# Kernel tuning notes

Measured on AMD Instinct MI355X. Metric: run time of the kernel, lower is better.

Reference implementation:

```python
import jax, jax.numpy as jnp
import numpy as np

NUM_HEADS = 16
HEAD_DIM = 128
ROTARY_DIM = 32  # head_dim * rotary_pct(0.25)
ROPE_BASE = 10000.0
SCALE = HEAD_DIM ** -0.5


def _rotate_half(x):
    x1, x2 = jnp.split(x, 2, axis=-1)
    return jnp.concatenate((-x2, x1), axis=-1)


def _rope_tables(seq_len, dtype):
    inv_freq = 1.0 / (ROPE_BASE ** (jnp.arange(0, ROTARY_DIM, 2, dtype=jnp.float32) / ROTARY_DIM))
    freqs = jnp.arange(seq_len, dtype=jnp.float32)[:, None] * inv_freq[None, :]  # [S, rd/2]
    emb = jnp.concatenate((freqs, freqs), axis=-1)  # [S, rd]
    return jnp.cos(emb).astype(dtype), jnp.sin(emb).astype(dtype)


def setup_inputs() -> dict:
    key = jax.random.key(0)
    k1, k2, k3 = jax.random.split(key, 3)
    B, S, H = 2, 2048, 2048
    hidden_states = jax.random.normal(k1, (B, S, H), dtype=jnp.float32)
    attention_mask = jnp.zeros((B, 1, S, S), dtype=jnp.float32)
    Wqkv = jax.random.normal(k2, (H, 3 * H), dtype=jnp.float32) * (H ** -0.5)
    Wout = jax.random.normal(k3, (H, H), dtype=jnp.float32) * (H ** -0.5)
    return {"hidden_states": hidden_states, "attention_mask": attention_mask,
            "Wqkv": Wqkv, "Wout": Wout}


def reference(hidden_states, attention_mask, Wqkv, Wout):
    B, S, H = hidden_states.shape
    qkv = jnp.einsum('bsh,hk->bsk', hidden_states, Wqkv)  # [B,S,3H]
    q, k, v = jnp.split(qkv, 3, axis=-1)

    def to_heads(x):
        return x.reshape(B, S, NUM_HEADS, HEAD_DIM).transpose(0, 2, 1, 3)  # [B,nh,S,hd]

    q, k, v = to_heads(q), to_heads(k), to_heads(v)

    cos, sin = _rope_tables(S, hidden_states.dtype)  # [S, ROTARY_DIM]
    cos = cos[None, None, :, :]
    sin = sin[None, None, :, :]

    def rope(x):
        xr = x[..., :ROTARY_DIM]
        xr = xr * cos + _rotate_half(xr) * sin
        return jnp.concatenate((xr, x[..., ROTARY_DIM:]), axis=-1)

    q, k = rope(q), rope(k)

    scores = jnp.einsum('bhqd,bhkd->bhqk', q, k) * SCALE + attention_mask
    probs = jax.nn.softmax(scores, axis=-1)  # dropout p=0 -> identity
    ctx = jnp.einsum('bhqk,bhkd->bhqd', probs, v)
    ctx = ctx.transpose(0, 2, 1, 3).reshape(B, S, H)
    return jnp.einsum('bsh,ho->bso', ctx, Wout)
```

## Files before the change

kernel.cpp:

```cpp
#include <hip/hip_runtime.h>

typedef __attribute__((ext_vector_type(4))) float f32x4;
typedef __attribute__((ext_vector_type(8))) short s16x8;
typedef __attribute__((ext_vector_type(4))) unsigned short u16x4;
typedef __attribute__((ext_vector_type(8))) unsigned short u16x8;

#define DEVINL __device__ __forceinline__

constexpr int Bb = 2;
constexpr int Ss = 2048;
constexpr int Hh = 2048;
constexpr int NH = 16;
constexpr int HD = 128;
constexpr float ATT_SCALE = 0.08838834764831845f;
constexpr float CEXP = ATT_SCALE * 1.44269504089f;
constexpr float INV_SCALE = 11.313708498984761f;
constexpr float RAW_THR = 90.50966799f;

DEVINL unsigned short f2bf(float f) {
    unsigned u = __float_as_uint(f);
    u += 0x7FFFu + ((u >> 16) & 1u);
    return (unsigned short)(u >> 16);
}
DEVINL float bf2f(unsigned short h) { return __uint_as_float(((unsigned)h) << 16); }
DEVINL float fexp2(float x) { return __builtin_amdgcn_exp2f(x); }

DEVINL void gl16(const void* g, void* l) {
    __builtin_amdgcn_global_load_lds((const __attribute__((address_space(1))) void*)g,
                                     (__attribute__((address_space(3))) void*)l, 16, 0, 0);
}

__global__ void zero_flag_k(int* f) { if (threadIdx.x == 0) *f = 0; }

__global__ void scan_mask_k(const float* __restrict__ m, int* __restrict__ flag) {
    size_t i = ((size_t)blockIdx.x * 256 + threadIdx.x) * 4;
    f32x4 v = *(const f32x4*)(m + i);
    int any = (v[0] != 0.f) || (v[1] != 0.f) || (v[2] != 0.f) || (v[3] != 0.f);
    if (__any(any)) { if ((threadIdx.x & 63) == 0) atomicOr(flag, 1); }
}

__global__ void convH_k(const float* __restrict__ x, unsigned short* __restrict__ y) {
    size_t i = (size_t)blockIdx.x * 256 + threadIdx.x;
    f32x4 a = *(const f32x4*)(x + i * 8);
    f32x4 b = *(const f32x4*)(x + i * 8 + 4);
    u16x8 o;
    o[0] = f2bf(a[0]); o[1] = f2bf(a[1]); o[2] = f2bf(a[2]); o[3] = f2bf(a[3]);
    o[4] = f2bf(b[0]); o[5] = f2bf(b[1]); o[6] = f2bf(b[2]); o[7] = f2bf(b[3]);
    *(u16x8*)(y + i * 8) = o;
}

__global__ void convT_k(const float* __restrict__ W, unsigned short* __restrict__ Wt,
                        int R, int C) {
    __shared__ float tile[32][33];
    int c0 = blockIdx.x * 32, r0 = blockIdx.y * 32;
    int t = threadIdx.x;
    int rr = t >> 3, cc = (t & 7) * 4;
    f32x4 v = *(const f32x4*)(W + (size_t)(r0 + rr) * C + c0 + cc);
    tile[rr][cc + 0] = v[0]; tile[rr][cc + 1] = v[1];
    tile[rr][cc + 2] = v[2]; tile[rr][cc + 3] = v[3];
    __syncthreads();
    u16x4 o;
    o[0] = f2bf(tile[cc + 0][rr]); o[1] = f2bf(tile[cc + 1][rr]);
    o[2] = f2bf(tile[cc + 2][rr]); o[3] = f2bf(tile[cc + 3][rr]);
    *(u16x4*)(Wt + (size_t)(c0 + rr) * R + r0 + cc) = o;
}

template<int MODE>
__global__ __launch_bounds__(256)
void gemm_bt_k(const unsigned short* __restrict__ A, const unsigned short* __restrict__ Bt,
               float* __restrict__ Cf, unsigned short* __restrict__ Cb,
               int M, int N, int K) {
    __shared__ char lds[128 * 64 * 2 * 2];
    char* As = lds;
    char* Bs = lds + 128 * 64 * 2;
    int t = threadIdx.x, w = t >> 6, ln = t & 63, lr = ln & 15, lg = ln >> 4;
    int f = blockIdx.x;
    int cpx = gridDim.x >> 3;
    int s = (f & 7) * cpx + (f >> 3);
    int nbn = N >> 7;
    int nb = s % nbn, mb = s / nbn;
    int m0 = mb * 128, n0 = nb * 128;
    int wr = w >> 1, wc = w & 1;
    const char* Abt = (const char*)A;
    const char* Bbt = (const char*)Bt;

    f32x4 acc[4][4];
#pragma unroll
    for (int i = 0; i < 4; ++i)
#pragma unroll
        for (int j = 0; j < 4; ++j) { acc[i][j][0] = 0.f; acc[i][j][1] = 0.f; acc[i][j][2] = 0.f; acc[i][j][3] = 0.f; }

    for (int k0 = 0; k0 < K; k0 += 64) {
        __syncthreads();
#pragma unroll
        for (int vv = 0; vv < 4; ++vv) {
            int ci = vv * 256 + t;
            int row = ci >> 3, cb = (ci & 7) << 4;
            int sc = cb ^ ((row & 7) << 4);
            gl16(Abt + ((size_t)(m0 + row) * K + k0) * 2 + sc, As + ci * 16);
            gl16(Bbt + ((size_t)(n0 + row) * K + k0) * 2 + sc, Bs + ci * 16);
        }
        __syncthreads();
#pragma unroll
        for (int kc = 0; kc < 2; ++kc) {
            s16x8 af[4], bfr[4];
#pragma unroll
            for (int i = 0; i < 4; ++i) {
                int rowa = wr * 64 + i * 16 + lr;
                af[i] = *(const s16x8*)(As + rowa * 128 + ((kc * 64 + lg * 16) ^ ((rowa & 7) << 4)));
                int rowb = wc * 64 + i * 16 + lr;
                bfr[i] = *(const s16x8*)(Bs + rowb * 128 + ((kc * 64 + lg * 16) ^ ((rowb & 7) << 4)));
            }
#pragma unroll
            for (int i = 0; i < 4; ++i)
#pragma unroll
                for (int j = 0; j < 4; ++j)
                    acc[i][j] = __builtin_amdgcn_mfma_f32_16x16x32_bf16(af[i], bfr[j], acc[i][j], 0, 0, 0);
        }
    }

    if (MODE == 0 && n0 < 4096 && wc == 0) {
        float invf = fexp2((float)lr * -0.83048202372f);
#pragma unroll
        for (int i = 0; i < 4; ++i)
#pragma unroll
            for (int r = 0; r < 4; ++r) {
                int srow = (m0 + wr * 64 + i * 16 + lg * 4 + r) & (Ss - 1);
                float sn, cs;
                sincosf((float)srow * invf, &sn, &cs);
                float x1 = acc[i][0][r], x2 = acc[i][1][r];
                acc[i][0][r] = x1 * cs - x2 * sn;
                acc[i][1][r] = x2 * cs + x1 * sn;
            }
    }

#pragma unroll
    for (int i = 0; i < 4; ++i)
#pragma unroll
        for (int j = 0; j < 4; ++j)
#pragma unroll
            for (int r = 0; r < 4; ++r) {
                int gr = m0 + wr * 64 + i * 16 + lg * 4 + r;
                int gc = n0 + wc * 64 + j * 16 + lr;
                float vv = acc[i][j][r];
                if (MODE == 1) Cf[(size_t)gr * N + gc] = vv;
                else           Cb[(size_t)gr * N + gc] = f2bf(vv);
            }
}

__global__ void vtrans_k(const unsigned short* __restrict__ qkv, unsigned short* __restrict__ Vt) {
    __shared__ unsigned short tile[64][40];
    int bh = blockIdx.x; int b = bh >> 4, h = bh & 15;
    int s0 = blockIdx.y * 64, d0 = blockIdx.z * 32;
    int t = threadIdx.x;
    int r = t >> 2, c8 = (t & 3) * 8;
    u16x8 v = *(const u16x8*)(qkv + ((size_t)(b * Ss + s0 + r)) * 6144 + 4096 + h * 128 + d0 + c8);
#pragma unroll
    for (int e = 0; e < 8; ++e) tile[r][c8 + e] = v[e];
    __syncthreads();
    int dr = t >> 3, sc = (t & 7) * 8;
    u16x8 o;
#pragma unroll
    for (int e = 0; e < 8; ++e) o[e] = tile[sc + e][dr];
    *(u16x8*)(Vt + ((size_t)bh * HD + d0 + dr) * Ss + s0 + sc) = o;
}

__global__ __launch_bounds__(512)
void attn_k(const unsigned short* __restrict__ qkv, const unsigned short* __restrict__ Vt,
            const float* __restrict__ mask, unsigned short* __restrict__ ctxb,
            const int* __restrict__ flag) {
    __shared__ char ldsK[64 * 256];
    __shared__ char ldsV[128 * 128];
    __shared__ unsigned short ldsP[8][1024];
    int f = blockIdx.x;
    int swzb = (f & 7) * 64 + (f >> 3);
    int bh = swzb >> 4, qt = swzb & 15;
    int b = bh >> 4, h = bh & 15;
    int t = threadIdx.x, w = t >> 6, ln = t & 63, lr = ln & 15, lg = ln >> 4;
    int useMask = *flag;
    int qw0 = qt * 128 + w * 16;
    const char* qkvB = (const char*)qkv;
    const char* VtB = (const char*)Vt;

    s16x8 qf[4];
    size_t qbase = ((size_t)(b * Ss + qw0 + lr)) * 6144 + h * 128;
#pragma unroll
    for (int kc = 0; kc < 4; ++kc) qf[kc] = *(const s16x8*)(qkv + qbase + kc * 32 + lg * 8);

    float mr = -3e38f, lsum = 0.f;
    f32x4 ctxa[8];
#pragma unroll
    for (int dn = 0; dn < 8; ++dn) { ctxa[dn][0] = 0.f; ctxa[dn][1] = 0.f; ctxa[dn][2] = 0.f; ctxa[dn][3] = 0.f; }
    const float* mrow = mask + (size_t)b * Ss * Ss;

    for (int kk0 = 0; kk0 < Ss; kk0 += 64) {
        __syncthreads();
#pragma unroll
        for (int c = 0; c < 2; ++c) {
            int ci = c * 512 + t;
            int krow = ci >> 4, kcb = (ci & 15) << 4;
            gl16(qkvB + (((size_t)(b * Ss + kk0 + krow)) * 6144 + 2048 + h * 128) * 2 + (kcb ^ ((krow & 7) << 4)),
                 ldsK + ci * 16);
            int vrow = ci >> 3, vcb = (ci & 7) << 4;
            gl16(VtB + (((size_t)(bh * 128 + vrow)) * 2048 + kk0) * 2 + (vcb ^ ((vrow & 7) << 4)),
                 ldsV + ci * 16);
        }
        __syncthreads();

        f32x4 st[4];
#pragma unroll
        for (int n = 0; n < 4; ++n) {
            f32x4 sacc = {0.f, 0.f, 0.f, 0.f};
            const char* kb = ldsK + (n * 16 + lr) * 256;
            int sw = (lr & 7) << 4;
#pragma unroll
            for (int kc = 0; kc < 4; ++kc) {
                s16x8 kf = *(const s16x8*)(kb + ((kc * 64 + lg * 16) ^ sw));
                sacc = __builtin_amdgcn_mfma_f32_16x16x32_bf16(kf, qf[kc], sacc, 0, 0, 0);
            }
            st[n] = sacc;
        }
        if (useMask) {
#pragma unroll
            for (int n = 0; n < 4; ++n)
#pragma unroll
                for (int r = 0; r < 4; ++r)
                    st[n][r] += mrow[(size_t)(qw0 + lr) * Ss + kk0 + n * 16 + lg * 4 + r] * INV_SCALE;
        }
        float pmax = st[0][0];
#pragma unroll
        for (int n = 0; n < 4; ++n)
#pragma unroll
            for (int r = 0; r < 4; ++r) pmax = fmaxf(pmax, st[n][r]);
        pmax = fmaxf(pmax, __shfl_xor(pmax, 16));
        pmax = fmaxf(pmax, __shfl_xor(pmax, 32));
        bool need = pmax > mr + RAW_THR;
        if (__any(need)) {
            float mn = fmaxf(mr, pmax);
            float al = fexp2((mr - mn) * CEXP);
            mr = mn;
            lsum *= al;
            float a0 = __shfl(al, lg * 4 + 0), a1 = __shfl(al, lg * 4 + 1);
            float a2 = __shfl(al, lg * 4 + 2), a3 = __shfl(al, lg * 4 + 3);
#pragma unroll
            for (int dn = 0; dn < 8; ++dn) {
                ctxa[dn][0] *= a0; ctxa[dn][1] *= a1; ctxa[dn][2] *= a2; ctxa[dn][3] *= a3;
            }
        }
        float mC = mr * CEXP;
        float rs = 0.f;
        u16x4 pk[4];
#pragma unroll
        for (int n = 0; n < 4; ++n)
#pragma unroll
            for (int r = 0; r < 4; ++r) {
                float p = fexp2(st[n][r] * CEXP - mC);
                rs += p;
                pk[n][r] = f2bf(p);
            }
        rs += __shfl_xor(rs, 16);
        rs += __shfl_xor(rs, 32);
        lsum += rs;
        char* pw = (char*)ldsP[w];
        int swp = (lr & 7) << 4;
#pragma unroll
        for (int n = 0; n < 4; ++n)
            *(u16x4*)(pw + lr * 128 + ((32 * n + 8 * lg) ^ swp)) = pk[n];
        asm volatile("s_waitcnt lgkmcnt(0)" ::: "memory");
        s16x8 pa[2];
#pragma unroll
        for (int c2 = 0; c2 < 2; ++c2)
            pa[c2] = *(const s16x8*)(pw + lr * 128 + ((64 * c2 + 16 * lg) ^ swp));
#pragma unroll
        for (int dn = 0; dn < 8; ++dn) {
            const char* vb = ldsV + (dn * 16 + lr) * 128;
#pragma unroll
            for (int c2 = 0; c2 < 2; ++c2) {
                s16x8 vf = *(const s16x8*)(vb + ((c2 * 64 + lg * 16) ^ swp));
                ctxa[dn] = __builtin_amdgcn_mfma_f32_16x16x32_bf16(pa[c2], vf, ctxa[dn], 0, 0, 0);
            }
        }
    }
    float l0 = 1.f / __shfl(lsum, lg * 4 + 0), l1 = 1.f / __shfl(lsum, lg * 4 + 1);
    float l2 = 1.f / __shfl(lsum, lg * 4 + 2), l3 = 1.f / __shfl(lsum, lg * 4 + 3);
#pragma unroll
    for (int dn = 0; dn < 8; ++dn) {
        size_t base = ((size_t)(b * Ss + qw0)) * Hh + h * 128 + dn * 16 + lr;
        ctxb[base + (size_t)(lg * 4 + 0) * Hh] = f2bf(ctxa[dn][0] * l0);
        ctxb[base + (size_t)(lg * 4 + 1) * Hh] = f2bf(ctxa[dn][1] * l1);
        ctxb[base + (size_t)(lg * 4 + 2) * Hh] = f2bf(ctxa[dn][2] * l2);
        ctxb[base + (size_t)(lg * 4 + 3) * Hh] = f2bf(ctxa[dn][3] * l3);
    }
}

extern "C" void kernel_launch(void* const* d_in, const int* in_sizes, int n_in,
                              void* d_out, int out_size, void* d_ws, size_t ws_size,
                              hipStream_t stream) {
    (void)in_sizes; (void)n_in; (void)out_size; (void)ws_size;
    const float* hidden = (const float*)d_in[0];
    const float* mask   = (const float*)d_in[1];
    const float* Wqkv   = (const float*)d_in[2];
    const float* Wout   = (const float*)d_in[3];
    float* out = (float*)d_out;

    char* ws = (char*)d_ws;
    size_t off = 0;
    auto alloc = [&](size_t bytes) { char* p = ws + off; off += (bytes + 255) & ~(size_t)255; return p; };
    unsigned short* hbf   = (unsigned short*)alloc((size_t)8388608 * 2);
    unsigned short* wqkvT = (unsigned short*)alloc((size_t)12582912 * 2);
    unsigned short* woutT = (unsigned short*)alloc((size_t)4194304 * 2);
    unsigned short* qkv   = (unsigned short*)alloc((size_t)25165824 * 2);
    unsigned short* Vt    = (unsigned short*)alloc((size_t)8388608 * 2);
    int* flag             = (int*)alloc(256);
    unsigned short* ctx = hbf;

    zero_flag_k<<<1, 64, 0, stream>>>(flag);
    scan_mask_k<<<2048, 256, 0, stream>>>(mask, flag);
    convH_k<<<4096, 256, 0, stream>>>(hidden, hbf);
    convT_k<<<dim3(192, 64), 256, 0, stream>>>(Wqkv, wqkvT, 2048, 6144);
    convT_k<<<dim3(64, 64), 256, 0, stream>>>(Wout, woutT, 2048, 2048);
    gemm_bt_k<0><<<1536, 256, 0, stream>>>(hbf, wqkvT, nullptr, qkv, 4096, 6144, 2048);
    vtrans_k<<<dim3(32, 32, 4), 256, 0, stream>>>(qkv, Vt);
    attn_k<<<512, 512, 0, stream>>>(qkv, Vt, mask, ctx, flag);
    gemm_bt_k<1><<<512, 256, 0, stream>>>(ctx, woutT, out, nullptr, 4096, 2048, 2048);
}
```

Measured before the change: 314.8 us.

## Use 256x256 double-buffered GEMM tiles with overlapped global-to-LDS loads

Replaces the 128x128 single-buffered GEMM with a 256x256 tile kernel using 512 threads. It double-buffers LDS at 128KB and issues the next K-tile's global loads while the current MFMAs run, with explicit waitcnt, barriers and setprio around the MFMA bursts. This aims to raise data reuse per tile and hide memory latency behind compute. In exchange, the grids shrink to 384 and 128 blocks, which risks wave-quantization tails and leaves many CUs idle for the output projection. The large LDS footprint also limits each CU to one block.

```diff
diff --git a/kernel.cpp b/kernel.cpp
--- a/kernel.cpp
+++ b/kernel.cpp
@@ -66,66 +66,114 @@
 }
 
 template<int MODE>
-__global__ __launch_bounds__(256)
-void gemm_bt_k(const unsigned short* __restrict__ A, const unsigned short* __restrict__ Bt,
+__global__ __launch_bounds__(512, 2)
+void gemm256_k(const unsigned short* __restrict__ A, const unsigned short* __restrict__ Bt,
                float* __restrict__ Cf, unsigned short* __restrict__ Cb,
                int M, int N, int K) {
-    __shared__ char lds[128 * 64 * 2 * 2];
-    char* As = lds;
-    char* Bs = lds + 128 * 64 * 2;
+    __shared__ char lds[131072];
     int t = threadIdx.x, w = t >> 6, ln = t & 63, lr = ln & 15, lg = ln >> 4;
-    int f = blockIdx.x;
-    int cpx = gridDim.x >> 3;
+    int wm = w >> 2, wn = w & 3;
+    int f = blockIdx.x, cpx = gridDim.x >> 3;
     int s = (f & 7) * cpx + (f >> 3);
-    int nbn = N >> 7;
+    int nbn = N >> 8;
     int nb = s % nbn, mb = s / nbn;
-    int m0 = mb * 128, n0 = nb * 128;
-    int wr = w >> 1, wc = w & 1;
-    const char* Abt = (const char*)A;
-    const char* Bbt = (const char*)Bt;
-
-    f32x4 acc[4][4];
-#pragma unroll
-    for (int i = 0; i < 4; ++i)
+    int m0 = mb * 256, n0 = nb * 256;
+    const char* Ab = (const char*)A;
+    const char* Bbp = (const char*)Bt;
+
+    f32x4 acc[8][4];
+#pragma unroll
+    for (int i = 0; i < 8; ++i)
 #pragma unroll
         for (int j = 0; j < 4; ++j) { acc[i][j][0] = 0.f; acc[i][j][1] = 0.f; acc[i][j][2] = 0.f; acc[i][j][3] = 0.f; }
 
-    for (int k0 = 0; k0 < K; k0 += 64) {
-        __syncthreads();
-#pragma unroll
-        for (int vv = 0; vv < 4; ++vv) {
-            int ci = vv * 256 + t;
+    auto STAGE = [&](int buf, int kt) {
+        size_t k0 = (size_t)kt * 64;
+        char* dA = lds + buf * 65536;
+        char* dB = dA + 32768;
+#pragma unroll
+        for (int ld = 0; ld < 4; ++ld) {
+            int ci = ld * 512 + t;
             int row = ci >> 3, cb = (ci & 7) << 4;
             int sc = cb ^ ((row & 7) << 4);
-            gl16(Abt + ((size_t)(m0 + row) * K + k0) * 2 + sc, As + ci * 16);
-            gl16(Bbt + ((size_t)(n0 + row) * K + k0) * 2 + sc, Bs + ci * 16);
-        }
-        __syncthreads();
-#pragma unroll
-        for (int kc = 0; kc < 2; ++kc) {
-            s16x8 af[4], bfr[4];
-#pragma unroll
-            for (int i = 0; i < 4; ++i) {
-                int rowa = wr * 64 + i * 16 + lr;
-                af[i] = *(const s16x8*)(As + rowa * 128 + ((kc * 64 + lg * 16) ^ ((rowa & 7) << 4)));
-                int rowb = wc * 64 + i * 16 + lr;
-                bfr[i] = *(const s16x8*)(Bs + rowb * 128 + ((kc * 64 + lg * 16) ^ ((rowb & 7) << 4)));
-            }
-#pragma unroll
-            for (int i = 0; i < 4; ++i)
+            gl16(Ab + ((size_t)(m0 + row) * K + k0) * 2 + sc, dA + ci * 16);
+        }
+#pragma unroll
+        for (int ld = 0; ld < 4; ++ld) {
+            int ci = ld * 512 + t;
+            int row = ci >> 3, cb = (ci & 7) << 4;
+            int sc = cb ^ ((row & 7) << 4);
+            gl16(Bbp + ((size_t)(n0 + row) * K + k0) * 2 + sc, dB + ci * 16);
+        }
+    };
+
+    const int NT = K >> 6;
+    STAGE(0, 0);
+    STAGE(1, 1);
+
+    for (int it = 0; it < (NT >> 1); ++it) {
+        int e = 2 * it;
+#pragma unroll
+        for (int half = 0; half < 2; ++half) {
+            const char* Ax = lds + half * 65536;
+            const char* Bx = Ax + 32768;
+            asm volatile("s_waitcnt vmcnt(8)" ::: "memory");
+            __builtin_amdgcn_s_barrier();
+            __builtin_amdgcn_sched_barrier(0);
+            s16x8 af[8], bfr[4];
+#pragma unroll
+            for (int i = 0; i < 8; ++i) {
+                int rowa = wm * 128 + i * 16 + lr;
+                af[i] = *(const s16x8*)(Ax + rowa * 128 + ((lg * 16) ^ ((rowa & 7) << 4)));
+            }
+#pragma unroll
+            for (int j = 0; j < 4; ++j) {
+                int rowb = wn * 64 + j * 16 + lr;
+                bfr[j] = *(const s16x8*)(Bx + rowb * 128 + ((lg * 16) ^ ((rowb & 7) << 4)));
+            }
+            asm volatile("s_waitcnt lgkmcnt(0)" ::: "memory");
+            __builtin_amdgcn_sched_barrier(0);
+            __builtin_amdgcn_s_setprio(1);
+#pragma unroll
+            for (int i = 0; i < 8; ++i)
 #pragma unroll
                 for (int j = 0; j < 4; ++j)
                     acc[i][j] = __builtin_amdgcn_mfma_f32_16x16x32_bf16(af[i], bfr[j], acc[i][j], 0, 0, 0);
+            __builtin_amdgcn_s_setprio(0);
+#pragma unroll
+            for (int i = 0; i < 8; ++i) {
+                int rowa = wm * 128 + i * 16 + lr;
+                af[i] = *(const s16x8*)(Ax + rowa * 128 + ((64 + lg * 16) ^ ((rowa & 7) << 4)));
+            }
+#pragma unroll
+            for (int j = 0; j < 4; ++j) {
+                int rowb = wn * 64 + j * 16 + lr;
+                bfr[j] = *(const s16x8*)(Bx + rowb * 128 + ((64 + lg * 16) ^ ((rowb & 7) << 4)));
+            }
+            asm volatile("s_waitcnt lgkmcnt(0)" ::: "memory");
+            __builtin_amdgcn_sched_barrier(0);
+            __builtin_amdgcn_s_barrier();
+            __builtin_amdgcn_sched_barrier(0);
+            int stg = e + 2 + half;
+            if (stg >= NT) stg -= 2;
+            STAGE(half, stg);
+            __builtin_amdgcn_s_setprio(1);
+#pragma unroll
+            for (int i = 0; i < 8; ++i)
+#pragma unroll
+                for (int j = 0; j < 4; ++j)
+                    acc[i][j] = __builtin_amdgcn_mfma_f32_16x16x32_bf16(af[i], bfr[j], acc[i][j], 0, 0, 0);
+            __builtin_amdgcn_s_setprio(0);
         }
     }
 
-    if (MODE == 0 && n0 < 4096 && wc == 0) {
+    if (MODE == 0 && n0 < 4096 && (wn & 1) == 0) {
         float invf = fexp2((float)lr * -0.83048202372f);
 #pragma unroll
-        for (int i = 0; i < 4; ++i)
+        for (int i = 0; i < 8; ++i)
 #pragma unroll
             for (int r = 0; r < 4; ++r) {
-                int srow = (m0 + wr * 64 + i * 16 + lg * 4 + r) & (Ss - 1);
+                int srow = (m0 + wm * 128 + i * 16 + lg * 4 + r) & (Ss - 1);
                 float sn, cs;
                 sincosf((float)srow * invf, &sn, &cs);
                 float x1 = acc[i][0][r], x2 = acc[i][1][r];
@@ -135,13 +183,13 @@
     }
 
 #pragma unroll
-    for (int i = 0; i < 4; ++i)
+    for (int i = 0; i < 8; ++i)
 #pragma unroll
         for (int j = 0; j < 4; ++j)
 #pragma unroll
             for (int r = 0; r < 4; ++r) {
-                int gr = m0 + wr * 64 + i * 16 + lg * 4 + r;
-                int gc = n0 + wc * 64 + j * 16 + lr;
+                int gr = m0 + wm * 128 + i * 16 + lg * 4 + r;
+                int gc = n0 + wn * 64 + j * 16 + lr;
                 float vv = acc[i][j][r];
                 if (MODE == 1) Cf[(size_t)gr * N + gc] = vv;
                 else           Cb[(size_t)gr * N + gc] = f2bf(vv);
@@ -319,8 +367,8 @@
     convH_k<<<4096, 256, 0, stream>>>(hidden, hbf);
     convT_k<<<dim3(192, 64), 256, 0, stream>>>(Wqkv, wqkvT, 2048, 6144);
     convT_k<<<dim3(64, 64), 256, 0, stream>>>(Wout, woutT, 2048, 2048);
-    gemm_bt_k<0><<<1536, 256, 0, stream>>>(hbf, wqkvT, nullptr, qkv, 4096, 6144, 2048);
+    gemm256_k<0><<<384, 512, 0, stream>>>(hbf, wqkvT, nullptr, qkv, 4096, 6144, 2048);
     vtrans_k<<<dim3(32, 32, 4), 256, 0, stream>>>(qkv, Vt);
     attn_k<<<512, 512, 0, stream>>>(qkv, Vt, mask, ctx, flag);
-    gemm_bt_k<1><<<512, 256, 0, stream>>>(ctx, woutT, out, nullptr, 4096, 2048, 2048);
-}
+    gemm256_k<1><<<128, 512, 0, stream>>>(ctx, woutT, out, nullptr, 4096, 2048, 2048);
+}
```

Measured after the change: 315.1 us. Within noise of the previous version (+0.1%).

## Replace QKV projection GEMM with 256x256-tile pipelined kernel

Applied to the files above, without the earlier changes.

Adds a new GEMM kernel using 256x256 output tiles, 512 threads and a double-buffered LDS pipeline. Global-to-LDS loads for upcoming K-slices are interleaved with MFMA phases under explicit waitcnt, barriers and priority hints. It is used for the QKV projection with the fused RoPE epilogue, replacing the 128x128 kernel. The aim is more operand reuse per byte loaded and better overlap of memory and compute. The cost is heavy register and LDS pressure (128 KB LDS, launch_bounds 512,2) and only 384 blocks, which can hurt occupancy or tail balance.

```diff
diff --git a/kernel.cpp b/kernel.cpp
--- a/kernel.cpp
+++ b/kernel.cpp
@@ -63,6 +63,127 @@
     o[0] = f2bf(tile[cc + 0][rr]); o[1] = f2bf(tile[cc + 1][rr]);
     o[2] = f2bf(tile[cc + 2][rr]); o[3] = f2bf(tile[cc + 3][rr]);
     *(u16x4*)(Wt + (size_t)(c0 + rr) * R + r0 + cc) = o;
+}
+
+#define PH(buf, kh, ih, sbuf, sX, skh, st, vm)                                    \
+  {                                                                               \
+    const char* Ar = lds + (buf)*65536 + (kh)*16384;                              \
+    const char* Br = lds + (buf)*65536 + 32768 + (kh)*16384;                      \
+    s16x8 af[4];                                                                  \
+    if ((ih) == 0) {                                                              \
+      _Pragma("unroll")                                                           \
+      for (int j = 0; j < 4; ++j)                                                 \
+        bfr[j] = *(const s16x8*)(Br + (wn*64 + j*16 + lr)*64 + lg*16);            \
+    }                                                                             \
+    _Pragma("unroll")                                                             \
+    for (int i = 0; i < 4; ++i)                                                   \
+      af[i] = *(const s16x8*)(Ar + (wm*128 + (ih)*64 + i*16 + lr)*64 + lg*16);    \
+    STG(sbuf, sX, skh, st);                                                       \
+    __builtin_amdgcn_s_barrier();                                                 \
+    __builtin_amdgcn_sched_barrier(0);                                            \
+    asm volatile("s_waitcnt lgkmcnt(0)" ::: "memory");                            \
+    __builtin_amdgcn_sched_barrier(0);                                            \
+    __builtin_amdgcn_s_setprio(1);                                                \
+    _Pragma("unroll")                                                             \
+    for (int i = 0; i < 4; ++i)                                                   \
+      _Pragma("unroll")                                                           \
+      for (int j = 0; j < 4; ++j)                                                 \
+        acc[(ih)*4 + i][j] = __builtin_amdgcn_mfma_f32_16x16x32_bf16(             \
+            af[i], bfr[j], acc[(ih)*4 + i][j], 0, 0, 0);                          \
+    __builtin_amdgcn_s_setprio(0);                                                \
+    if ((vm) == 8) { asm volatile("s_waitcnt vmcnt(8)" ::: "memory"); }           \
+    if ((vm) == 4) { asm volatile("s_waitcnt vmcnt(4)" ::: "memory"); }           \
+    __builtin_amdgcn_sched_barrier(0);                                            \
+    __builtin_amdgcn_s_barrier();                                                 \
+    __builtin_amdgcn_sched_barrier(0);                                            \
+  }
+
+template<int MODE>
+__global__ __launch_bounds__(512, 2)
+void gemm256_k(const unsigned short* __restrict__ A, const unsigned short* __restrict__ Bt,
+               float* __restrict__ Cf, unsigned short* __restrict__ Cb,
+               int M, int N, int K) {
+    __shared__ char lds[131072];
+    int t = threadIdx.x, w = t >> 6, ln = t & 63, lr = ln & 15, lg = ln >> 4;
+    int wm = w >> 2, wn = w & 3;
+    int f = blockIdx.x, cpx = gridDim.x >> 3;
+    int s = (f & 7) * cpx + (f >> 3);
+    int nbn = N >> 8;
+    int nb = s % nbn, mb = s / nbn;
+    int m0 = mb * 256, n0 = nb * 256;
+    const char* Ab = (const char*)A;
+    const char* Bbp = (const char*)Bt;
+
+    f32x4 acc[8][4];
+#pragma unroll
+    for (int i = 0; i < 8; ++i)
+#pragma unroll
+        for (int j = 0; j < 4; ++j) { acc[i][j][0] = 0.f; acc[i][j][1] = 0.f; acc[i][j][2] = 0.f; acc[i][j][3] = 0.f; }
+
+    auto STG = [&](int sbuf, int sX, int skh, int kt) {
+        char* dst = lds + sbuf * 65536 + sX * 32768 + skh * 16384;
+        const char* src = sX ? Bbp : Ab;
+        int rbase = sX ? n0 : m0;
+        size_t kcol = (size_t)kt * 64 + skh * 32;
+#pragma unroll
+        for (int ld = 0; ld < 2; ++ld) {
+            int ci = ld * 512 + t;
+            int row = ci >> 2, sl = ci & 3;
+            gl16(src + ((size_t)(rbase + row) * K + kcol) * 2 + sl * 16, dst + ci * 16);
+        }
+    };
+
+    const int NT = K >> 6;
+    STG(0, 0, 0, 0); STG(0, 1, 0, 0); STG(0, 0, 1, 0); STG(0, 1, 1, 0);
+    STG(1, 0, 0, 1); STG(1, 1, 0, 1);
+    asm volatile("s_waitcnt vmcnt(4)" ::: "memory");
+    __builtin_amdgcn_sched_barrier(0);
+    __builtin_amdgcn_s_barrier();
+    __builtin_amdgcn_sched_barrier(0);
+
+    s16x8 bfr[4];
+    for (int it = 0; it < (NT >> 1); ++it) {
+        int e = it * 2;
+        int t2 = (e + 2 < NT) ? e + 2 : e;
+        int t3 = (e + 3 < NT) ? e + 3 : e + 1;
+        PH(0, 0, 0,  1, 0, 1, e + 1, 0)
+        PH(0, 0, 1,  1, 1, 1, e + 1, 0)
+        PH(0, 1, 0,  0, 0, 0, t2,    0)
+        PH(0, 1, 1,  0, 1, 0, t2,    8)
+        PH(1, 0, 0,  0, 0, 1, t2,    0)
+        PH(1, 0, 1,  0, 1, 1, t2,    8)
+        PH(1, 1, 0,  1, 0, 0, t3,    0)
+        PH(1, 1, 1,  1, 1, 0, t3,    4)
+    }
+    asm volatile("s_waitcnt vmcnt(0)" ::: "memory");
+
+    if (MODE == 0 && n0 < 4096 && (wn & 1) == 0) {
+        float invf = fexp2((float)lr * -0.83048202372f);
+#pragma unroll
+        for (int i = 0; i < 8; ++i)
+#pragma unroll
+            for (int r = 0; r < 4; ++r) {
+                int srow = (m0 + wm * 128 + i * 16 + lg * 4 + r) & (Ss - 1);
+                float sn, cs;
+                sincosf((float)srow * invf, &sn, &cs);
+                float x1 = acc[i][0][r], x2 = acc[i][1][r];
+                acc[i][0][r] = x1 * cs - x2 * sn;
+                acc[i][1][r] = x2 * cs + x1 * sn;
+            }
+    }
+
+#pragma unroll
+    for (int i = 0; i < 8; ++i)
+#pragma unroll
+        for (int j = 0; j < 4; ++j)
+#pragma unroll
+            for (int r = 0; r < 4; ++r) {
+                int gr = m0 + wm * 128 + i * 16 + lg * 4 + r;
+                int gc = n0 + wn * 64 + j * 16 + lr;
+                float vv = acc[i][j][r];
+                if (MODE == 1) Cf[(size_t)gr * N + gc] = vv;
+                else           Cb[(size_t)gr * N + gc] = f2bf(vv);
+            }
 }
 
 template<int MODE>
@@ -118,22 +239,6 @@
                     acc[i][j] = __builtin_amdgcn_mfma_f32_16x16x32_bf16(af[i], bfr[j], acc[i][j], 0, 0, 0);
         }
     }
-
-    if (MODE == 0 && n0 < 4096 && wc == 0) {
-        float invf = fexp2((float)lr * -0.83048202372f);
-#pragma unroll
-        for (int i = 0; i < 4; ++i)
-#pragma unroll
-            for (int r = 0; r < 4; ++r) {
-                int srow = (m0 + wr * 64 + i * 16 + lg * 4 + r) & (Ss - 1);
-                float sn, cs;
-                sincosf((float)srow * invf, &sn, &cs);
-                float x1 = acc[i][0][r], x2 = acc[i][1][r];
-                acc[i][0][r] = x1 * cs - x2 * sn;
-                acc[i][1][r] = x2 * cs + x1 * sn;
-            }
-    }
-
 #pragma unroll
     for (int i = 0; i < 4; ++i)
 #pragma unroll
@@ -319,7 +424,7 @@
     convH_k<<<4096, 256, 0, stream>>>(hidden, hbf);
     convT_k<<<dim3(192, 64), 256, 0, stream>>>(Wqkv, wqkvT, 2048, 6144);
     convT_k<<<dim3(64, 64), 256, 0, stream>>>(Wout, woutT, 2048, 2048);
-    gemm_bt_k<0><<<1536, 256, 0, stream>>>(hbf, wqkvT, nullptr, qkv, 4096, 6144, 2048);
+    gemm256_k<0><<<384, 512, 0, stream>>>(hbf, wqkvT, nullptr, qkv, 4096, 6144, 2048);
     vtrans_k<<<dim3(32, 32, 4), 256, 0, stream>>>(qkv, Vt);
     attn_k<<<512, 512, 0, stream>>>(qkv, Vt, mask, ctx, flag);
     gemm_bt_k<1><<<512, 256, 0, stream>>>(ctx, woutT, out, nullptr, 4096, 2048, 2048);
```

Measured after the change: 313.8 us. About the same (-0.3%).
